# Kernel tuning notes

Measured on AMD Instinct MI355X. Metric: run time of the kernel, lower is better.

Reference implementation:

```python
import jax, jax.numpy as jnp
import numpy as np

EPS = 1e-6
ROPE_BASE = 10000.0


def rms_norm(x, gamma):
    # normalize over last dim (head_dim)
    var = jnp.mean(x * x, axis=-1, keepdims=True)
    return x * jax.lax.rsqrt(var + EPS) * gamma


def apply_rope(x):
    # x: [B, L, nH, hd]; rotate-half RoPE over flattened sequence positions
    L, hd = x.shape[1], x.shape[-1]
    half = hd // 2
    inv_freq = 1.0 / (ROPE_BASE ** (jnp.arange(half, dtype=jnp.float32) / half))
    ang = jnp.arange(L, dtype=jnp.float32)[:, None] * inv_freq[None, :]  # [L, half]
    cos = jnp.cos(ang)[None, :, None, :]
    sin = jnp.sin(ang)[None, :, None, :]
    x1, x2 = x[..., :half], x[..., half:]
    return jnp.concatenate([x1 * cos - x2 * sin, x1 * sin + x2 * cos], axis=-1)


def setup_inputs() -> dict:
    key = jax.random.key(0)
    k1, k2, k3 = jax.random.split(key, 3)
    B, H, W, C = 8, 32, 32, 768
    x = jax.random.normal(k1, (B, H, W, C), dtype=jnp.float32)
    w_qkv = jax.random.normal(k2, (3 * C, C), dtype=jnp.float32) * (1.0 / np.sqrt(C))
    w_out = jax.random.normal(k3, (C, C), dtype=jnp.float32) * (1.0 / np.sqrt(C))
    q_gamma = jnp.ones((64,), dtype=jnp.float32)
    k_gamma = jnp.ones((64,), dtype=jnp.float32)
    return {"x": x, "w_qkv": w_qkv, "q_gamma": q_gamma, "k_gamma": k_gamma, "w_out": w_out}


def reference(x, w_qkv, q_gamma, k_gamma, w_out):
    B, H, W, C = x.shape
    nH = 12
    hd = C // nH
    L = H * W
    x_flat = x.reshape(B, L, C)
    qkv = jnp.einsum('blc,dc->bld', x_flat, w_qkv).reshape(B, L, 3, nH, hd)
    q, k, v = qkv[:, :, 0], qkv[:, :, 1], qkv[:, :, 2]  # [B, L, nH, hd]
    q = apply_rope(rms_norm(q, q_gamma))
    k = apply_rope(rms_norm(k, k_gamma))
    scale = 1.0 / np.sqrt(hd)
    scores = jnp.einsum('bqhd,bkhd->bhqk', q, k) * scale
    attn = jax.nn.softmax(scores, axis=-1)
    out = jnp.einsum('bhqk,bkhd->bqhd', attn, v).reshape(B, H, W, C)
    return jnp.einsum('bhwc,dc->bhwd', out, w_out)
```

## Files before the change

### kernel.cpp

```cpp
#include <hip/hip_runtime.h>
#include <math.h>

#define NB 8
#define SL 1024
#define CD 768
#define NHH 12
#define HD 64
#define QKVD 2304

typedef __attribute__((ext_vector_type(8))) __bf16 bf16x8;
typedef __attribute__((ext_vector_type(8))) unsigned short u16x8;
typedef __attribute__((ext_vector_type(4))) float f32x4;
typedef __attribute__((ext_vector_type(16))) float f32x16;
typedef __attribute__((ext_vector_type(4))) unsigned int u32x4;
#define MFMA16(a, b, c) __builtin_amdgcn_mfma_f32_16x16x32_bf16(a, b, c, 0, 0, 0)
#define MFMA32(a, b, c) __builtin_amdgcn_mfma_f32_32x32x16_bf16(a, b, c, 0, 0, 0)

__host__ __device__ __forceinline__ float bf2f(unsigned short u) {
  union { unsigned int i; float f; } v; v.i = ((unsigned int)u) << 16; return v.f;
}
__host__ __device__ __forceinline__ unsigned short f2bf(float f) {
  union { float ff; unsigned int i; } v; v.ff = f;
  unsigned int x = v.i;
  x += 0x7FFFu + ((x >> 16) & 1u);
  return (unsigned short)(x >> 16);
}
__device__ __forceinline__ unsigned int pkbf(float a, float b) {
  unsigned short ua = __builtin_bit_cast(unsigned short, (__bf16)a);
  unsigned short ub = __builtin_bit_cast(unsigned short, (__bf16)b);
  return ((unsigned int)ub << 16) | ua;
}

__device__ __forceinline__ void gload_lds16(const void* g, void* l) {
  __builtin_amdgcn_global_load_lds(
      (const __attribute__((address_space(1))) unsigned int*)g,
      (__attribute__((address_space(3))) unsigned int*)l, 16, 0, 0);
}

__global__ __launch_bounds__(256) void conv_kernel(
    const float4* __restrict__ in, ushort4* __restrict__ out, int n4)
{
  int i = blockIdx.x * 256 + threadIdx.x;
  if (i < n4) {
    float4 v = in[i];
    ushort4 o;
    o.x = f2bf(v.x); o.y = f2bf(v.y); o.z = f2bf(v.z); o.w = f2bf(v.w);
    out[i] = o;
  }
}

template <int MODE>
__global__ __launch_bounds__(256) void gemm_mfma(
    const unsigned short* __restrict__ A, const unsigned short* __restrict__ B,
    void* __restrict__ Cv, int M, int N, int K,
    const float* __restrict__ qg, const float* __restrict__ kg)
{
  __shared__ alignas(16) unsigned short AsL[128 * 32];
  __shared__ alignas(16) unsigned short BsL[128 * 32];
  const int m0 = blockIdx.y * 128, n0 = blockIdx.x * 128;
  const int t = threadIdx.x;
  const int wave = t >> 6, lane = t & 63;
  const int wm = (wave >> 1) * 64, wn = (wave & 1) * 64;
  const int lm = lane & 15, quad = lane >> 4;
  f32x4 acc[4][4];
#pragma unroll
  for (int i = 0; i < 4; ++i)
#pragma unroll
    for (int j = 0; j < 4; ++j)
#pragma unroll
      for (int r = 0; r < 4; ++r) acc[i][j][r] = 0.f;

  const int sr = t >> 2, sc = (t & 3) * 8;
  const unsigned short* ag = A + (size_t)(m0 + sr) * K + sc;
  const unsigned short* bg = B + (size_t)(n0 + sr) * K + sc;
  for (int k0 = 0; k0 < K; k0 += 32) {
    gload_lds16(ag + k0, &AsL[t * 8]);
    gload_lds16(ag + (size_t)64 * K + k0, &AsL[2048 + t * 8]);
    gload_lds16(bg + k0, &BsL[t * 8]);
    gload_lds16(bg + (size_t)64 * K + k0, &BsL[2048 + t * 8]);
    __syncthreads();
    bf16x8 af[4], bfr[4];
#pragma unroll
    for (int i = 0; i < 4; ++i)
      af[i] = *(const bf16x8*)&AsL[(wm + i * 16 + lm) * 32 + quad * 8];
#pragma unroll
    for (int j = 0; j < 4; ++j)
      bfr[j] = *(const bf16x8*)&BsL[(wn + j * 16 + lm) * 32 + quad * 8];
#pragma unroll
    for (int i = 0; i < 4; ++i)
#pragma unroll
      for (int j = 0; j < 4; ++j)
        acc[i][j] = MFMA16(af[i], bfr[j], acc[i][j]);
    __syncthreads();
  }

  if (MODE == 2 && (n0 + wn) < 2 * CD) {
    const float* gam = ((n0 + wn) >= CD) ? kg : qg;
    float g4[4];
#pragma unroll
    for (int j = 0; j < 4; ++j) g4[j] = gam[j * 16 + lm];
    const float C1 = -13.287712379549449f / 32.0f;
    const float if0 = exp2f((float)lm * C1);
    const float if1 = exp2f((float)(16 + lm) * C1);
    unsigned short* Cs = (unsigned short*)Cv;
#pragma unroll
    for (int i = 0; i < 4; ++i) {
      const int row = m0 + wm + i * 16 + quad * 4;
#pragma unroll
      for (int r = 0; r < 4; ++r) {
        float v0 = acc[i][0][r], v1 = acc[i][1][r];
        float v2 = acc[i][2][r], v3 = acc[i][3][r];
        float ssq = v0 * v0 + v1 * v1 + v2 * v2 + v3 * v3;
#pragma unroll
        for (int off = 8; off; off >>= 1) ssq += __shfl_xor(ssq, off);
        const float sc2 = rsqrtf(ssq * (1.0f / 64.0f) + 1e-6f);
        v0 *= sc2 * g4[0]; v1 *= sc2 * g4[1];
        v2 *= sc2 * g4[2]; v3 *= sc2 * g4[3];
        const int l = (row + r) & (SL - 1);
        float sn0, cs0, sn1, cs1;
        sincosf((float)l * if0, &sn0, &cs0);
        sincosf((float)l * if1, &sn1, &cs1);
        const size_t base = (size_t)(row + r) * N + n0 + wn + lm;
        Cs[base +  0] = f2bf(v0 * cs0 - v2 * sn0);
        Cs[base + 16] = f2bf(v1 * cs1 - v3 * sn1);
        Cs[base + 32] = f2bf(v0 * sn0 + v2 * cs0);
        Cs[base + 48] = f2bf(v1 * sn1 + v3 * cs1);
      }
    }
    return;
  }

#pragma unroll
  for (int i = 0; i < 4; ++i) {
    const int row = m0 + wm + i * 16 + quad * 4;
#pragma unroll
    for (int r = 0; r < 4; ++r) {
      const size_t base = (size_t)(row + r) * N + n0 + wn + lm;
#pragma unroll
      for (int j = 0; j < 4; ++j) {
        if (MODE == 1) ((float*)Cv)[base + j * 16] = acc[i][j][r];
        else ((unsigned short*)Cv)[base + j * 16] = f2bf(acc[i][j][r]);
      }
    }
  }
}

__global__ __launch_bounds__(256) void attn_mfma(
    const unsigned short* __restrict__ qkv, unsigned short* __restrict__ ctx)
{
  __shared__ alignas(16) unsigned short KsL[2][64 * 64];
  __shared__ alignas(16) unsigned short Vt[2][64][76];
  const int bid = (int)(blockIdx.x + 8 * (blockIdx.y + 12 * blockIdx.z));
  const int nb = (bid & 7) * 96 + (bid >> 3);
  const int qt = nb & 7;
  const int h = (nb >> 3) % 12;
  const int b = nb / 96;
  const int t = threadIdx.x, wave = t >> 6, lane = t & 63;
  const int q_l = lane & 31, hi = lane >> 5;
  const int wq = wave * 32;
  const int vkey = t & 63, vds = (t >> 6) * 16;
  const int kr = t >> 3, kc = t & 7;
  const float SCALE = 0.125f * 1.44269504088896340736f;

  const unsigned short* base_k = qkv + (size_t)b * SL * QKVD + (NHH * HD) + h * HD;
  const unsigned short* base_v = qkv + (size_t)b * SL * QKVD + 2 * (NHH * HD) + h * HD;

  bf16x8 qf[4];
  {
    const unsigned short* qp =
        qkv + (((size_t)(b * SL + qt * 128 + wq + q_l) * 3 + 0) * NHH + h) * HD + hi * 8;
#pragma unroll
    for (int ds = 0; ds < 4; ++ds) qf[ds] = *(const bf16x8*)(qp + ds * 16);
  }
  f32x16 o0, o1;
#pragma unroll
  for (int r = 0; r < 16; ++r) { o0[r] = 0.f; o1[r] = 0.f; }
  float m_i = -INFINITY, l_i = 0.f;

  const int ksw = (kc ^ (kr & 7)) * 8;
#define STAGE_K(KT, BUF)                                                      \
  {                                                                           \
    const unsigned short* k0p = base_k + (size_t)((KT)*64 + kr) * QKVD + ksw; \
    gload_lds16(k0p, &KsL[BUF][t * 8]);                                       \
    const unsigned short* k1p =                                               \
        base_k + (size_t)((KT)*64 + 32 + kr) * QKVD + ksw;                    \
    gload_lds16(k1p, &KsL[BUF][2048 + t * 8]);                                \
  }

  STAGE_K(0, 0);
  {
    const unsigned short* vp = base_v + (size_t)vkey * QKVD + vds;
    u16x8 v0 = *(const u16x8*)(vp);
    u16x8 v1 = *(const u16x8*)(vp + 8);
#pragma unroll
    for (int e = 0; e < 8; ++e) {
      Vt[0][vds + e][vkey] = v0[e];
      Vt[0][vds + 8 + e][vkey] = v1[e];
    }
  }
  __syncthreads();

  for (int kt = 0; kt < 16; ++kt) {
    const int cur = kt & 1, nxt = cur ^ 1;
    const int ktn = (kt + 1) & 15;
    STAGE_K(ktn, nxt);
    const unsigned short* vp = base_v + (size_t)(ktn * 64 + vkey) * QKVD + vds;
    u16x8 v0n = *(const u16x8*)(vp);
    u16x8 v1n = *(const u16x8*)(vp + 8);
    const unsigned short* Kb = KsL[cur];
    f32x16 st0, st1;
#pragma unroll
    for (int r = 0; r < 16; ++r) { st0[r] = 0.f; st1[r] = 0.f; }
    __builtin_amdgcn_s_setprio(1);
#pragma unroll
    for (int ds = 0; ds < 4; ++ds) {
      const int c = 2 * ds + hi;
      bf16x8 k0 = *(const bf16x8*)&Kb[q_l * 64 + ((c ^ (q_l & 7)) * 8)];
      bf16x8 k1 = *(const bf16x8*)&Kb[(32 + q_l) * 64 + ((c ^ (q_l & 7)) * 8)];
      st0 = MFMA32(k0, qf[ds], st0);
      st1 = MFMA32(k1, qf[ds], st1);
    }
    __builtin_amdgcn_s_setprio(0);
    float t0 = fmaxf(st0[0], st1[0]), t1 = fmaxf(st0[1], st1[1]);
    float t2 = fmaxf(st0[2], st1[2]), t3 = fmaxf(st0[3], st1[3]);
#pragma unroll
    for (int r = 4; r < 16; r += 4) {
      t0 = fmaxf(t0, fmaxf(st0[r + 0], st1[r + 0]));
      t1 = fmaxf(t1, fmaxf(st0[r + 1], st1[r + 1]));
      t2 = fmaxf(t2, fmaxf(st0[r + 2], st1[r + 2]));
      t3 = fmaxf(t3, fmaxf(st0[r + 3], st1[r + 3]));
    }
    float tm = fmaxf(fmaxf(t0, t1), fmaxf(t2, t3)) * SCALE;
    tm = fmaxf(tm, __shfl_xor(tm, 32));
    if (!__all(tm - m_i <= 8.0f)) {
      const float mn = fmaxf(m_i, tm);
      const float al = __builtin_amdgcn_exp2f(m_i - mn);
      m_i = mn;
      l_i *= al;
#pragma unroll
      for (int r = 0; r < 16; ++r) { o0[r] *= al; o1[r] *= al; }
    }
    float rs = 0.f;
#pragma unroll
    for (int r = 0; r < 16; ++r) {
      st0[r] = __builtin_amdgcn_exp2f(fmaf(st0[r], SCALE, -m_i));
      st1[r] = __builtin_amdgcn_exp2f(fmaf(st1[r], SCALE, -m_i));
      rs += st0[r] + st1[r];
    }
    rs += __shfl_xor(rs, 32);
    l_i += rs;
#define PV_KS(KS, PVEC, RL)                                              \
    {                                                                    \
      unsigned int a0 = pkbf(PVEC[RL + 0], PVEC[RL + 1]);                \
      unsigned int a1 = pkbf(PVEC[RL + 2], PVEC[RL + 3]);                \
      unsigned int b0 = pkbf(PVEC[RL + 4], PVEC[RL + 5]);                \
      unsigned int b1 = pkbf(PVEC[RL + 6], PVEC[RL + 7]);                \
      unsigned int s0 = hi ? a0 : b0, s1 = hi ? a1 : b1;                 \
      unsigned int r0 = __shfl_xor(s0, 32), r1 = __shfl_xor(s1, 32);     \
      u32x4 pw;                                                          \
      pw[0] = hi ? r0 : a0; pw[1] = hi ? r1 : a1;                        \
      pw[2] = hi ? b0 : r0; pw[3] = hi ? b1 : r1;                        \
      bf16x8 paf = __builtin_bit_cast(bf16x8, pw);                       \
      bf16x8 v0f = *(const bf16x8*)&Vt[cur][q_l][(KS)*16 + hi * 8];      \
      bf16x8 v1f = *(const bf16x8*)&Vt[cur][32 + q_l][(KS)*16 + hi * 8]; \
      __builtin_amdgcn_s_setprio(1);                                     \
      o0 = MFMA32(v0f, paf, o0);                                         \
      o1 = MFMA32(v1f, paf, o1);                                         \
      __builtin_amdgcn_s_setprio(0);                                     \
    }
    PV_KS(0, st0, 0)
    PV_KS(1, st0, 8)
    PV_KS(2, st1, 0)
    PV_KS(3, st1, 8)
#undef PV_KS
#pragma unroll
    for (int e = 0; e < 8; ++e) {
      Vt[nxt][vds + e][vkey] = v0n[e];
      Vt[nxt][vds + 8 + e][vkey] = v1n[e];
    }
    __syncthreads();
  }
  const float inv = 1.f / l_i;
  const size_t row = (size_t)(b * SL + qt * 128 + wq + q_l) * CD + h * HD;
#pragma unroll
  for (int g = 0; g < 4; ++g) {
    uint2 w0, w1;
    w0.x = pkbf(o0[4 * g + 0] * inv, o0[4 * g + 1] * inv);
    w0.y = pkbf(o0[4 * g + 2] * inv, o0[4 * g + 3] * inv);
    *(uint2*)&ctx[row + 8 * g + 4 * hi] = w0;
    w1.x = pkbf(o1[4 * g + 0] * inv, o1[4 * g + 1] * inv);
    w1.y = pkbf(o1[4 * g + 2] * inv, o1[4 * g + 3] * inv);
    *(uint2*)&ctx[row + 32 + 8 * g + 4 * hi] = w1;
  }
#undef STAGE_K
}

extern "C" void kernel_launch(void* const* d_in, const int* in_sizes, int n_in,
                              void* d_out, int out_size, void* d_ws, size_t ws_size,
                              hipStream_t stream) {
  const float* x     = (const float*)d_in[0];
  const float* w_qkv = (const float*)d_in[1];
  const float* qg    = (const float*)d_in[2];
  const float* kg    = (const float*)d_in[3];
  const float* w_out = (const float*)d_in[4];

  unsigned short* xb  = (unsigned short*)d_ws;
  unsigned short* wqb = xb + (size_t)NB * SL * CD;
  unsigned short* wob = wqb + (size_t)QKVD * CD;
  unsigned short* qkv = wob + (size_t)CD * CD;
  unsigned short* ctx = qkv + (size_t)NB * SL * QKVD;

  const int M = NB * SL;
  dim3 blk(256);
  conv_kernel<<<dim3(M * CD / 4 / 256), blk, 0, stream>>>(
      (const float4*)x, (ushort4*)xb, M * CD / 4);
  conv_kernel<<<dim3(QKVD * CD / 4 / 256), blk, 0, stream>>>(
      (const float4*)w_qkv, (ushort4*)wqb, QKVD * CD / 4);
  conv_kernel<<<dim3(CD * CD / 4 / 256), blk, 0, stream>>>(
      (const float4*)w_out, (ushort4*)wob, CD * CD / 4);
  gemm_mfma<2><<<dim3(QKVD / 128, M / 128), blk, 0, stream>>>(
      xb, wqb, qkv, M, QKVD, CD, qg, kg);
  attn_mfma<<<dim3(SL / 128, NHH, NB), blk, 0, stream>>>(qkv, ctx);
  gemm_mfma<1><<<dim3(CD / 128, M / 128), blk, 0, stream>>>(
      ctx, wob, d_out, M, CD, CD, nullptr, nullptr);
}
```

Before: 244.8 us.

## Double-buffer GEMM LDS loads, swizzle LDS, remap blocks, precompute RoPE table

The GEMM kernel now double-buffers its LDS tiles so the global-to-LDS loads for the next K step are issued before the current step's MFMAs, and drops one barrier per iteration. It also XOR-swizzles the LDS column layout to cut bank conflicts, remaps block IDs across 8 groups for XCD-friendly L2 locality, and raises wave priority around the MFMA block. RoPE sin/cos values come from a precomputed table built by a new small kernel instead of per-element sincosf. LDS use doubles, which may reduce occupancy, and the table adds one extra launch.

```diff
diff --git a/kernel.cpp b/kernel.cpp
--- a/kernel.cpp
+++ b/kernel.cpp
@@ -49,19 +49,35 @@
   }
 }
 
+__global__ __launch_bounds__(256) void rope_tab_kernel(float2* __restrict__ rt)
+{
+  int i = blockIdx.x * 256 + threadIdx.x;
+  int l = i >> 5, j = i & 31;
+  float ang = (float)l * exp2f((float)j * (-13.287712379549449f / 32.0f));
+  float sn, cs;
+  sincosf(ang, &sn, &cs);
+  rt[i] = make_float2(cs, sn);
+}
+
 template <int MODE>
 __global__ __launch_bounds__(256) void gemm_mfma(
     const unsigned short* __restrict__ A, const unsigned short* __restrict__ B,
     void* __restrict__ Cv, int M, int N, int K,
-    const float* __restrict__ qg, const float* __restrict__ kg)
+    const float* __restrict__ qg, const float* __restrict__ kg,
+    const float2* __restrict__ rt)
 {
-  __shared__ alignas(16) unsigned short AsL[128 * 32];
-  __shared__ alignas(16) unsigned short BsL[128 * 32];
-  const int m0 = blockIdx.y * 128, n0 = blockIdx.x * 128;
+  __shared__ alignas(16) unsigned short AsL[2][128 * 32];
+  __shared__ alignas(16) unsigned short BsL[2][128 * 32];
+  const int bid = (int)(blockIdx.x + gridDim.x * blockIdx.y);
+  const int cpx = (int)(gridDim.x * gridDim.y) >> 3;
+  const int nb = (bid & 7) * cpx + (bid >> 3);
+  const int bx = nb % (int)gridDim.x, by = nb / (int)gridDim.x;
+  const int m0 = by * 128, n0 = bx * 128;
   const int t = threadIdx.x;
   const int wave = t >> 6, lane = t & 63;
   const int wm = (wave >> 1) * 64, wn = (wave & 1) * 64;
   const int lm = lane & 15, quad = lane >> 4;
+  const int rq = (quad ^ ((lm >> 1) & 3)) * 8;
   f32x4 acc[4][4];
 #pragma unroll
   for (int i = 0; i < 4; ++i)
@@ -70,38 +86,47 @@
 #pragma unroll
       for (int r = 0; r < 4; ++r) acc[i][j][r] = 0.f;
 
-  const int sr = t >> 2, sc = (t & 3) * 8;
-  const unsigned short* ag = A + (size_t)(m0 + sr) * K + sc;
-  const unsigned short* bg = B + (size_t)(n0 + sr) * K + sc;
+  const int sr = t >> 2, kc4 = t & 3;
+  const int scs = (kc4 ^ ((sr >> 1) & 3)) * 8;
+  const unsigned short* ag = A + (size_t)(m0 + sr) * K + scs;
+  const unsigned short* bg = B + (size_t)(n0 + sr) * K + scs;
+#define STAGE_G(K0, BUF)                                          \
+  {                                                               \
+    gload_lds16(ag + (K0), &AsL[BUF][t * 8]);                     \
+    gload_lds16(ag + (size_t)64 * K + (K0), &AsL[BUF][2048 + t * 8]); \
+    gload_lds16(bg + (K0), &BsL[BUF][t * 8]);                     \
+    gload_lds16(bg + (size_t)64 * K + (K0), &BsL[BUF][2048 + t * 8]); \
+  }
+
+  STAGE_G(0, 0);
+  __syncthreads();
+  int cur = 0;
   for (int k0 = 0; k0 < K; k0 += 32) {
-    gload_lds16(ag + k0, &AsL[t * 8]);
-    gload_lds16(ag + (size_t)64 * K + k0, &AsL[2048 + t * 8]);
-    gload_lds16(bg + k0, &BsL[t * 8]);
-    gload_lds16(bg + (size_t)64 * K + k0, &BsL[2048 + t * 8]);
-    __syncthreads();
+    if (k0 + 32 < K) STAGE_G(k0 + 32, cur ^ 1);
     bf16x8 af[4], bfr[4];
 #pragma unroll
     for (int i = 0; i < 4; ++i)
-      af[i] = *(const bf16x8*)&AsL[(wm + i * 16 + lm) * 32 + quad * 8];
+      af[i] = *(const bf16x8*)&AsL[cur][(wm + i * 16 + lm) * 32 + rq];
 #pragma unroll
     for (int j = 0; j < 4; ++j)
-      bfr[j] = *(const bf16x8*)&BsL[(wn + j * 16 + lm) * 32 + quad * 8];
+      bfr[j] = *(const bf16x8*)&BsL[cur][(wn + j * 16 + lm) * 32 + rq];
+    __builtin_amdgcn_s_setprio(1);
 #pragma unroll
     for (int i = 0; i < 4; ++i)
 #pragma unroll
       for (int j = 0; j < 4; ++j)
         acc[i][j] = MFMA16(af[i], bfr[j], acc[i][j]);
+    __builtin_amdgcn_s_setprio(0);
     __syncthreads();
-  }
+    cur ^= 1;
+  }
+#undef STAGE_G
 
   if (MODE == 2 && (n0 + wn) < 2 * CD) {
     const float* gam = ((n0 + wn) >= CD) ? kg : qg;
     float g4[4];
 #pragma unroll
     for (int j = 0; j < 4; ++j) g4[j] = gam[j * 16 + lm];
-    const float C1 = -13.287712379549449f / 32.0f;
-    const float if0 = exp2f((float)lm * C1);
-    const float if1 = exp2f((float)(16 + lm) * C1);
     unsigned short* Cs = (unsigned short*)Cv;
 #pragma unroll
     for (int i = 0; i < 4; ++i) {
@@ -117,14 +142,13 @@
         v0 *= sc2 * g4[0]; v1 *= sc2 * g4[1];
         v2 *= sc2 * g4[2]; v3 *= sc2 * g4[3];
         const int l = (row + r) & (SL - 1);
-        float sn0, cs0, sn1, cs1;
-        sincosf((float)l * if0, &sn0, &cs0);
-        sincosf((float)l * if1, &sn1, &cs1);
+        const float2 t0 = rt[l * 32 + lm];
+        const float2 t1 = rt[l * 32 + 16 + lm];
         const size_t base = (size_t)(row + r) * N + n0 + wn + lm;
-        Cs[base +  0] = f2bf(v0 * cs0 - v2 * sn0);
-        Cs[base + 16] = f2bf(v1 * cs1 - v3 * sn1);
-        Cs[base + 32] = f2bf(v0 * sn0 + v2 * cs0);
-        Cs[base + 48] = f2bf(v1 * sn1 + v3 * cs1);
+        Cs[base +  0] = f2bf(v0 * t0.x - v2 * t0.y);
+        Cs[base + 16] = f2bf(v1 * t1.x - v3 * t1.y);
+        Cs[base + 32] = f2bf(v0 * t0.y + v2 * t0.x);
+        Cs[base + 48] = f2bf(v1 * t1.y + v3 * t1.x);
       }
     }
     return;
@@ -309,6 +333,7 @@
   unsigned short* wob = wqb + (size_t)QKVD * CD;
   unsigned short* qkv = wob + (size_t)CD * CD;
   unsigned short* ctx = qkv + (size_t)NB * SL * QKVD;
+  float2* rtab = (float2*)(ctx + (size_t)NB * SL * CD);
 
   const int M = NB * SL;
   dim3 blk(256);
@@ -318,9 +343,10 @@
       (const float4*)w_qkv, (ushort4*)wqb, QKVD * CD / 4);
   conv_kernel<<<dim3(CD * CD / 4 / 256), blk, 0, stream>>>(
       (const float4*)w_out, (ushort4*)wob, CD * CD / 4);
+  rope_tab_kernel<<<dim3(SL * 32 / 256), blk, 0, stream>>>(rtab);
   gemm_mfma<2><<<dim3(QKVD / 128, M / 128), blk, 0, stream>>>(
-      xb, wqb, qkv, M, QKVD, CD, qg, kg);
+      xb, wqb, qkv, M, QKVD, CD, qg, kg, rtab);
   attn_mfma<<<dim3(SL / 128, NHH, NB), blk, 0, stream>>>(qkv, ctx);
   gemm_mfma<1><<<dim3(CD / 128, M / 128), blk, 0, stream>>>(
-      ctx, wob, d_out, M, CD, CD, nullptr, nullptr);
-}
+      ctx, wob, d_out, M, CD, CD, nullptr, nullptr, nullptr);
+}
```

Result: faster. 219.0 us (-10.6%).
